# Kernel optimization log

Hardware: AMD Instinct MI355X
Metric: run time of the kernel (lower is better)

## Reference

```python
import jax, jax.numpy as jnp
import numpy as np

K_DEFAULT = 1000.0  # torch.eye(3).fill_(1000.) fills ALL 9 entries, not just the diagonal
THRESH = 3.0
PENALTY = 10000.0


def setup_inputs() -> dict:
    key = jax.random.key(0)
    k1, k2, k3, k4, k5 = jax.random.split(key, 5)
    N, H, D, C = 2048, 128, 7, 64
    return {
        "start_state": jax.random.normal(k1, (1, D), dtype=jnp.float32),
        "state_batch": jax.random.normal(k2, (N, H, D), dtype=jnp.float32),
        "normals": jax.random.normal(k3, (C, 3), dtype=jnp.float32),
        "jac": jax.random.normal(k4, (C, 3, D), dtype=jnp.float32),
        "forces": jax.random.uniform(k5, (C,), dtype=jnp.float32),
    }


def reference(start_state, state_batch, normals, jac, forces):
    # k_c: torch.eye(3).fill_(1000.) => every entry 1000
    k_c = jnp.full((3, 3), K_DEFAULT, dtype=state_batch.dtype)
    # relative joint state: [N, H, 7]
    sb = state_batch[:, :, :7] - start_state[:, :7]
    # out[c, k] = normals[c, :] @ k_c @ jac[c, :, :]  -> [C, 7]
    out = jnp.einsum('ci,ij,cjk->ck', normals, k_c, jac)
    # deltas[n, h, c] = out[c, :] . sb[n, h, :]  (replaces the double Python loop)
    deltas = jnp.einsum('ck,nhk->nhc', out, sb)
    # fi[n, h] = sum_c (forces[c] + deltas[n, h, c])
    fi = jnp.sum(forces[None, None, :] + deltas, axis=2)
    cost = jnp.where(fi > THRESH, jnp.asarray(PENALTY, fi.dtype), jnp.zeros((), fi.dtype))
    return cost
```

## Files before the change

### kernel.cpp

```cpp
#include <hip/hip_runtime.h>


#define FTC_C 64
#define FTC_D 7

__global__ __launch_bounds__(256) void ForceThresholdCost_kernel(
    const float* __restrict__ start_state,
    const float* __restrict__ state_batch,
    const float* __restrict__ normals,
    const float* __restrict__ jac,
    const float* __restrict__ forces,
    float* __restrict__ out,
    int ntot)
{
    __shared__ double wpart[FTC_C][FTC_D];
    __shared__ double wred[FTC_D];
    __shared__ double fsum_s;
    __shared__ double bias_s;

    const int tid = threadIdx.x;

    if (tid < FTC_C) {
        double sn = (double)normals[tid * 3 + 0]
                  + (double)normals[tid * 3 + 1]
                  + (double)normals[tid * 3 + 2];
        #pragma unroll
        for (int k = 0; k < FTC_D; ++k) {
            double tk = (double)jac[tid * 21 + 0 * 7 + k]
                      + (double)jac[tid * 21 + 1 * 7 + k]
                      + (double)jac[tid * 21 + 2 * 7 + k];
            wpart[tid][k] = 1000.0 * sn * tk;
        }
    }
    __syncthreads();

    if (tid < FTC_D) {
        double s = 0.0;
        for (int c = 0; c < FTC_C; ++c) s += wpart[c][tid];
        wred[tid] = s;
    } else if (tid == FTC_D) {
        double f = 0.0;
        for (int c = 0; c < FTC_C; ++c) f += (double)forces[c];
        fsum_s = f;
    }
    __syncthreads();

    if (tid == 0) {
        double b = fsum_s;
        #pragma unroll
        for (int k = 0; k < FTC_D; ++k) b -= wred[k] * (double)start_state[k];
        bias_s = b;
    }
    __syncthreads();

    double w0 = wred[0], w1 = wred[1], w2 = wred[2], w3 = wred[3];
    double w4 = wred[4], w5 = wred[5], w6 = wred[6];
    double bias = bias_s;

    int idx = blockIdx.x * 256 + tid;
    if (idx < ntot) {
        const float* sp = state_batch + (size_t)idx * FTC_D;
        double fi = bias;
        fi = fma((double)sp[0], w0, fi);
        fi = fma((double)sp[1], w1, fi);
        fi = fma((double)sp[2], w2, fi);
        fi = fma((double)sp[3], w3, fi);
        fi = fma((double)sp[4], w4, fi);
        fi = fma((double)sp[5], w5, fi);
        fi = fma((double)sp[6], w6, fi);
        out[idx] = (fi > 3.0) ? 10000.0f : 0.0f;
    }
}

extern "C" void kernel_launch(void* const* d_in, const int* in_sizes, int n_in,
                              void* d_out, int out_size, void* d_ws, size_t ws_size,
                              hipStream_t stream) {
    const float* start_state = (const float*)d_in[0];
    const float* state_batch = (const float*)d_in[1];
    const float* normals     = (const float*)d_in[2];
    const float* jac         = (const float*)d_in[3];
    const float* forces      = (const float*)d_in[4];
    float* out = (float*)d_out;

    int ntot = in_sizes[1] / FTC_D;
    int grid = (ntot + 255) / 256;

    ForceThresholdCost_kernel<<<grid, 256, 0, stream>>>(
        start_state, state_batch, normals, jac, forces, out, ntot);
}
```

Baseline: 69.14 us.

## Split weight setup into separate kernel and vectorize main pass with float4

Moves the per-block recomputation of the folded weights and bias into a one-block setup kernel that reduces with wave shuffles and writes them to workspace. The main kernel then reads those 8 doubles and handles four rows per thread using seven float4 loads and one float4 store. This removes the three block barriers and the redundant setup work from every block, and widens the memory accesses. It costs an extra kernel launch and assumes the row count is a multiple of four, since any remainder rows are left unwritten.

```diff
diff --git a/kernel.cpp b/kernel.cpp
--- a/kernel.cpp
+++ b/kernel.cpp
@@ -1,74 +1,80 @@
 #include <hip/hip_runtime.h>
 
 
-#define FTC_C 64
 #define FTC_D 7
 
-__global__ __launch_bounds__(256) void ForceThresholdCost_kernel(
+__global__ __launch_bounds__(64) void ftc_setup_kernel(
     const float* __restrict__ start_state,
-    const float* __restrict__ state_batch,
     const float* __restrict__ normals,
     const float* __restrict__ jac,
     const float* __restrict__ forces,
+    double* __restrict__ wb)
+{
+    const int c = threadIdx.x;
+    double sn = (double)normals[c * 3 + 0]
+              + (double)normals[c * 3 + 1]
+              + (double)normals[c * 3 + 2];
+    double vals[8];
+    #pragma unroll
+    for (int k = 0; k < FTC_D; ++k) {
+        double tk = (double)jac[c * 21 + 0 * 7 + k]
+                  + (double)jac[c * 21 + 1 * 7 + k]
+                  + (double)jac[c * 21 + 2 * 7 + k];
+        vals[k] = 1000.0 * sn * tk;
+    }
+    vals[7] = (double)forces[c];
+
+    #pragma unroll
+    for (int off = 32; off > 0; off >>= 1) {
+        #pragma unroll
+        for (int k = 0; k < 8; ++k)
+            vals[k] += __shfl_xor(vals[k], off, 64);
+    }
+
+    if (c == 0) {
+        double b = vals[7];
+        #pragma unroll
+        for (int k = 0; k < FTC_D; ++k) b -= vals[k] * (double)start_state[k];
+        #pragma unroll
+        for (int k = 0; k < FTC_D; ++k) wb[k] = vals[k];
+        wb[7] = b;
+    }
+}
+
+__global__ __launch_bounds__(256) void ftc_main_kernel(
+    const float* __restrict__ state_batch,
+    const double* __restrict__ wb,
     float* __restrict__ out,
-    int ntot)
+    int nquad)
 {
-    __shared__ double wpart[FTC_C][FTC_D];
-    __shared__ double wred[FTC_D];
-    __shared__ double fsum_s;
-    __shared__ double bias_s;
+    double w0 = wb[0], w1 = wb[1], w2 = wb[2], w3 = wb[3];
+    double w4 = wb[4], w5 = wb[5], w6 = wb[6];
+    double bias = wb[7];
 
-    const int tid = threadIdx.x;
+    int t = blockIdx.x * 256 + threadIdx.x;
+    if (t < nquad) {
+        const float4* p = (const float4*)(state_batch + (size_t)t * 28);
+        float v[28];
+        float4* vv = (float4*)v;
+        #pragma unroll
+        for (int j = 0; j < 7; ++j) vv[j] = p[j];
 
-    if (tid < FTC_C) {
-        double sn = (double)normals[tid * 3 + 0]
-                  + (double)normals[tid * 3 + 1]
-                  + (double)normals[tid * 3 + 2];
+        float4 o;
+        float* ov = &o.x;
         #pragma unroll
-        for (int k = 0; k < FTC_D; ++k) {
-            double tk = (double)jac[tid * 21 + 0 * 7 + k]
-                      + (double)jac[tid * 21 + 1 * 7 + k]
-                      + (double)jac[tid * 21 + 2 * 7 + k];
-            wpart[tid][k] = 1000.0 * sn * tk;
+        for (int r = 0; r < 4; ++r) {
+            const float* s = v + r * 7;
+            double fi = bias;
+            fi = fma((double)s[0], w0, fi);
+            fi = fma((double)s[1], w1, fi);
+            fi = fma((double)s[2], w2, fi);
+            fi = fma((double)s[3], w3, fi);
+            fi = fma((double)s[4], w4, fi);
+            fi = fma((double)s[5], w5, fi);
+            fi = fma((double)s[6], w6, fi);
+            ov[r] = (fi > 3.0) ? 10000.0f : 0.0f;
         }
-    }
-    __syncthreads();
-
-    if (tid < FTC_D) {
-        double s = 0.0;
-        for (int c = 0; c < FTC_C; ++c) s += wpart[c][tid];
-        wred[tid] = s;
-    } else if (tid == FTC_D) {
-        double f = 0.0;
-        for (int c = 0; c < FTC_C; ++c) f += (double)forces[c];
-        fsum_s = f;
-    }
-    __syncthreads();
-
-    if (tid == 0) {
-        double b = fsum_s;
-        #pragma unroll
-        for (int k = 0; k < FTC_D; ++k) b -= wred[k] * (double)start_state[k];
-        bias_s = b;
-    }
-    __syncthreads();
-
-    double w0 = wred[0], w1 = wred[1], w2 = wred[2], w3 = wred[3];
-    double w4 = wred[4], w5 = wred[5], w6 = wred[6];
-    double bias = bias_s;
-
-    int idx = blockIdx.x * 256 + tid;
-    if (idx < ntot) {
-        const float* sp = state_batch + (size_t)idx * FTC_D;
-        double fi = bias;
-        fi = fma((double)sp[0], w0, fi);
-        fi = fma((double)sp[1], w1, fi);
-        fi = fma((double)sp[2], w2, fi);
-        fi = fma((double)sp[3], w3, fi);
-        fi = fma((double)sp[4], w4, fi);
-        fi = fma((double)sp[5], w5, fi);
-        fi = fma((double)sp[6], w6, fi);
-        out[idx] = (fi > 3.0) ? 10000.0f : 0.0f;
+        ((float4*)out)[t] = o;
     }
 }
 
@@ -81,10 +87,12 @@
     const float* jac         = (const float*)d_in[3];
     const float* forces      = (const float*)d_in[4];
     float* out = (float*)d_out;
+    double* wb = (double*)d_ws;
 
-    int ntot = in_sizes[1] / FTC_D;
-    int grid = (ntot + 255) / 256;
+    int ntot  = in_sizes[1] / FTC_D;
+    int nquad = ntot / 4;
+    int grid  = (nquad + 255) / 256;
 
-    ForceThresholdCost_kernel<<<grid, 256, 0, stream>>>(
-        start_state, state_batch, normals, jac, forces, out, ntot);
+    ftc_setup_kernel<<<1, 64, 0, stream>>>(start_state, normals, jac, forces, wb);
+    ftc_main_kernel<<<grid, 256, 0, stream>>>(state_batch, wb, out, nquad);
 }
```

New measurement: 67.73 us. 2.0% less time.
